# Kernel optimization log

Hardware: AMD Instinct MI355X
Metric: run time of the kernel (lower is better)

Reference implementation:

```python
import jax, jax.numpy as jnp
import numpy as np

NUM_HEADS = 4
NUM_GROUPS = 32
EPS = 1e-5

def setup_inputs() -> dict:
    key = jax.random.key(0)
    ks = jax.random.split(key, 3)
    B, C, H, W = 16, 512, 32, 32
    x = jax.random.normal(ks[0], (B, C, H, W), dtype=jnp.float32)
    gn_w = jnp.ones((C,), jnp.float32)
    gn_b = jnp.zeros((C,), jnp.float32)
    qkv_w = jax.random.normal(ks[1], (3 * C, C), dtype=jnp.float32) * (C ** -0.5)
    qkv_b = jnp.zeros((3 * C,), jnp.float32)
    proj_w = jax.random.normal(ks[2], (C, C), dtype=jnp.float32) * (C ** -0.5)
    proj_b = jnp.zeros((C,), jnp.float32)
    return {"x": x, "gn_w": gn_w, "gn_b": gn_b, "qkv_w": qkv_w,
            "qkv_b": qkv_b, "proj_w": proj_w, "proj_b": proj_b}

def group_norm(x, w, b):
    B, C, H, W = x.shape
    xg = x.reshape(B, NUM_GROUPS, C // NUM_GROUPS, H, W)
    mean = xg.mean(axis=(2, 3, 4), keepdims=True)
    var = xg.var(axis=(2, 3, 4), keepdims=True)
    xg = (xg - mean) * jax.lax.rsqrt(var + EPS)
    x = xg.reshape(B, C, H, W)
    return x * w[None, :, None, None] + b[None, :, None, None]

def reference(x, gn_w, gn_b, qkv_w, qkv_b, proj_w, proj_b):
    B, C, H, W = x.shape
    hd = C // NUM_HEADS
    h = group_norm(x, gn_w, gn_b)
    # 1x1 conv == channel matmul
    qkv = jnp.einsum('oc,bchw->bohw', qkv_w, h) + qkv_b[None, :, None, None]
    q, k, v = jnp.split(qkv, 3, axis=1)
    N = H * W
    q = q.reshape(B, NUM_HEADS, hd, N)
    k = k.reshape(B, NUM_HEADS, hd, N)
    v = v.reshape(B, NUM_HEADS, hd, N)
    scale = hd ** -0.5
    attn = jnp.einsum('bhcn,bhcm->bhnm', q, k) * scale
    attn = jax.nn.softmax(attn, axis=-1)
    o = jnp.einsum('bhnm,bhcm->bhcn', attn, v).reshape(B, C, H, W)
    o = jnp.einsum('oc,bchw->bohw', proj_w, o) + proj_b[None, :, None, None]
    return x + o
```

## Files before the change

kernel.cpp:

```cpp
#include <hip/hip_runtime.h>

typedef __attribute__((ext_vector_type(4))) float f32x4;
typedef __attribute__((ext_vector_type(8))) short s16x8;

#define MFMA16(a, b, c) __builtin_amdgcn_mfma_f32_16x16x32_bf16((a), (b), (c), 0, 0, 0)

__device__ __forceinline__ unsigned short f2bf(float f) {
    union { float f; unsigned u; } v; v.f = f;
    unsigned u = v.u + 0x7FFFu + ((v.u >> 16) & 1u);
    return (unsigned short)(u >> 16);
}

__device__ __forceinline__ unsigned cvtpk(float lo, float hi) {
    unsigned r;
    asm("v_cvt_pk_bf16_f32 %0, %1, %2" : "=v"(r) : "v"(lo), "v"(hi));
    return r;
}

__device__ __forceinline__ float exp2f_fast(float x) {
    float r;
    asm("v_exp_f32 %0, %1" : "=v"(r) : "v"(x));
    return r;
}

__device__ __forceinline__ void gll16(const unsigned short* g, unsigned short* l) {
    __builtin_amdgcn_global_load_lds((const __attribute__((address_space(1))) void*)g,
                                     (__attribute__((address_space(3))) void*)l, 16, 0, 0);
}

__global__ __launch_bounds__(256) void k_wconv(const float* __restrict__ qkv_w,
                                               const float* __restrict__ proj_w,
                                               unsigned short* __restrict__ wout) {
    int i = blockIdx.x * 256 + threadIdx.x;
    const int NQ = 3 * 512 * 512;
    float v = (i < NQ) ? qkv_w[i] : proj_w[i - NQ];
    wout[i] = f2bf(v);
}

__global__ __launch_bounds__(256) void k_gn(const float* __restrict__ x,
                                            const float* __restrict__ gnw,
                                            const float* __restrict__ gnb,
                                            unsigned short* __restrict__ h_t) {
    int bg = blockIdx.x;
    int b = bg >> 5, g = bg & 31;
    int t = threadIdx.x;
    const float4* p = (const float4*)(x + (size_t)bg * 16384);
    float s = 0.f, ss = 0.f;
    for (int i = t; i < 4096; i += 256) {
        float4 v = p[i];
        s += v.x + v.y + v.z + v.w;
        ss += v.x * v.x + v.y * v.y + v.z * v.z + v.w * v.w;
    }
    for (int w = 1; w < 64; w <<= 1) { s += __shfl_xor(s, w); ss += __shfl_xor(ss, w); }
    __shared__ float rs[4], rss[4], mv[2];
    __shared__ unsigned short ldt[1024][18];
    int wid = t >> 6;
    if ((t & 63) == 0) { rs[wid] = s; rss[wid] = ss; }
    __syncthreads();
    if (t == 0) {
        float S = rs[0] + rs[1] + rs[2] + rs[3];
        float SS = rss[0] + rss[1] + rss[2] + rss[3];
        float mean = S * (1.f / 16384.f);
        float var = SS * (1.f / 16384.f) - mean * mean;
        mv[0] = mean; mv[1] = rsqrtf(var + 1e-5f);
    }
    __syncthreads();
    int c = t >> 4, f4 = t & 15;
    float mean = mv[0], rstd = mv[1];
    float sc = gnw[g * 16 + c] * rstd;
    float sh = gnb[g * 16 + c] - mean * sc;
    const float4* pc = (const float4*)(x + ((size_t)(b * 512 + g * 16 + c)) * 1024);
#pragma unroll
    for (int i = 0; i < 16; ++i) {
        int n = i * 64 + f4 * 4;
        float4 v = pc[n >> 2];
        ldt[n + 0][c] = f2bf(v.x * sc + sh);
        ldt[n + 1][c] = f2bf(v.y * sc + sh);
        ldt[n + 2][c] = f2bf(v.z * sc + sh);
        ldt[n + 3][c] = f2bf(v.w * sc + sh);
    }
    __syncthreads();
    int half = t & 1;
#pragma unroll
    for (int i = 0; i < 8; ++i) {
        int row = i * 128 + (t >> 1);
        *(uint4*)(h_t + ((size_t)(b * 1024 + row)) * 512 + g * 16 + half * 8) =
            *(const uint4*)(&ldt[row][half * 8]);
    }
}

template<int MODE>
__global__ __launch_bounds__(512, 6) void k_gemm(const unsigned short* __restrict__ A,
                                                 const unsigned short* __restrict__ Bt,
                                                 const float* __restrict__ bias,
                                                 unsigned short* __restrict__ Qo,
                                                 unsigned short* __restrict__ Ko,
                                                 unsigned short* __restrict__ Vo,
                                                 const float* __restrict__ xres,
                                                 float* __restrict__ out) {
    const int Kd = 512;
    int id = blockIdx.x;
    int xcd = id & 7, j = id >> 3;
    int nt = xcd + 8 * (j & 15);
    int mt = j >> 4;
    int t = threadIdx.x, wid = t >> 6, lane = t & 63;
    int lm = lane & 15, q4 = lane >> 4;
    int wm = wid >> 2, wn = wid & 3;
    __shared__ unsigned short ldsA[2][4096];
    __shared__ unsigned short ldsB[2][4096];
    int m0 = mt * 128, n0 = nt * 128;

    int r = t >> 2;
    int cc = (t & 3) ^ (r & 3);
    const unsigned short* gA = A + (size_t)(m0 + r) * Kd + cc * 8;
    const unsigned short* gB = Bt + (size_t)(n0 + r) * Kd + cc * 8;
    unsigned short* dA[2] = { &ldsA[0][wid * 512], &ldsA[1][wid * 512] };
    unsigned short* dB[2] = { &ldsB[0][wid * 512], &ldsB[1][wid * 512] };

    f32x4 z = {0.f, 0.f, 0.f, 0.f};
    f32x4 acc[4][2];
#pragma unroll
    for (int fi = 0; fi < 4; ++fi)
#pragma unroll
        for (int fj = 0; fj < 2; ++fj) acc[fi][fj] = z;

    gll16(gA, dA[0]); gll16(gB, dB[0]);
    gA += 32; gB += 32;

    const int NK = 16;
    for (int ks = 0; ks < NK; ++ks) {
        int cur = ks & 1;
        if (ks + 1 < NK) {
            gll16(gA, dA[cur ^ 1]); gll16(gB, dB[cur ^ 1]);
            gA += 32; gB += 32;
            asm volatile("s_waitcnt vmcnt(2)" ::: "memory");
        } else {
            asm volatile("s_waitcnt vmcnt(0)" ::: "memory");
        }
        __builtin_amdgcn_s_barrier();
        asm volatile("" ::: "memory");
        const unsigned short* lA = ldsA[cur];
        const unsigned short* lB = ldsB[cur];
        s16x8 af[4], bg[2];
#pragma unroll
        for (int fi = 0; fi < 4; ++fi) {
            int rA = wm * 64 + fi * 16 + lm;
            af[fi] = *(const s16x8*)&lA[(rA * 4 + (q4 ^ (lm & 3))) * 8];
        }
#pragma unroll
        for (int fj = 0; fj < 2; ++fj) {
            int rB = wn * 32 + fj * 16 + lm;
            bg[fj] = *(const s16x8*)&lB[(rB * 4 + (q4 ^ (lm & 3))) * 8];
        }
        if (MODE == 0) {
#pragma unroll
            for (int fi = 0; fi < 4; ++fi)
#pragma unroll
                for (int fj = 0; fj < 2; ++fj) acc[fi][fj] = MFMA16(af[fi], bg[fj], acc[fi][fj]);
        } else {
#pragma unroll
            for (int fi = 0; fi < 4; ++fi)
#pragma unroll
                for (int fj = 0; fj < 2; ++fj) acc[fi][fj] = MFMA16(bg[fj], af[fi], acc[fi][fj]);
        }
        asm volatile("" ::: "memory");
        __builtin_amdgcn_s_barrier();
    }

    int b = nt >> 3;
    if (MODE == 0) {
        int part = mt >> 2;
        int head = mt & 3;
        int bh = b * 4 + head;
        const float qscale = 0.08838834764831845f * 1.4426950408889634f;
#pragma unroll
        for (int fi = 0; fi < 4; ++fi) {
            int ddb = wm * 64 + fi * 16 + 4 * q4;
            float bv[4];
#pragma unroll
            for (int i = 0; i < 4; ++i) bv[i] = bias[mt * 128 + ddb + i];
#pragma unroll
            for (int fj = 0; fj < 2; ++fj) {
                int n = ((nt & 7) << 7) + wn * 32 + fj * 16 + lm;
                f32x4 v = acc[fi][fj];
                uint2 pr;
                if (part == 0) {
                    pr.x = cvtpk((v[0] + bv[0]) * qscale, (v[1] + bv[1]) * qscale);
                    pr.y = cvtpk((v[2] + bv[2]) * qscale, (v[3] + bv[3]) * qscale);
                    *(uint2*)(Qo + ((size_t)bh * 1024 + n) * 128 + ddb) = pr;
                } else {
                    pr.x = cvtpk(v[0] + bv[0], v[1] + bv[1]);
                    pr.y = cvtpk(v[2] + bv[2], v[3] + bv[3]);
                    *(uint2*)(Ko + ((size_t)bh * 1024 + n) * 128 + ddb) = pr;
                }
            }
        }
    } else if (MODE == 1) {
        int bh = b * 4 + mt;
#pragma unroll
        for (int fi = 0; fi < 4; ++fi) {
            int d = wm * 64 + fi * 16 + lm;
            float bv = bias[mt * 128 + d];
#pragma unroll
            for (int fj = 0; fj < 2; ++fj) {
                int np = ((nt & 7) << 7) + wn * 32 + q4 * 8 + fj * 4;
                f32x4 v = acc[fi][fj];
                uint2 pr;
                pr.x = cvtpk(v[0] + bv, v[1] + bv);
                pr.y = cvtpk(v[2] + bv, v[3] + bv);
                *(uint2*)(Vo + ((size_t)bh * 128 + d) * 1024 + np) = pr;
            }
        }
    } else {
#pragma unroll
        for (int fi = 0; fi < 4; ++fi) {
            int oc = m0 + wm * 64 + fi * 16 + lm;
            float bv = bias[oc];
#pragma unroll
            for (int fj = 0; fj < 2; ++fj) {
                int n = ((nt & 7) << 7) + wn * 32 + fj * 16 + 4 * q4;
                size_t idx = ((size_t)b * 512 + oc) * 1024 + n;
                float4 xr = *(const float4*)&xres[idx];
                f32x4 v = acc[fi][fj];
                float4 o;
                o.x = xr.x + bv + v[0];
                o.y = xr.y + bv + v[1];
                o.z = xr.z + bv + v[2];
                o.w = xr.w + bv + v[3];
                *(float4*)&out[idx] = o;
            }
        }
    }
}

__global__ __launch_bounds__(256, 2) void k_attn(const unsigned short* __restrict__ Q,
                                                 const unsigned short* __restrict__ K,
                                                 const unsigned short* __restrict__ V,
                                                 unsigned short* __restrict__ o_t) {
    int id = blockIdx.y * 8 + blockIdx.x;
    int bh = (id & 7) + ((id >> 6) << 3);
    int qb = (id >> 3) & 7;
    int t = threadIdx.x, wid = t >> 6, lane = t & 63;
    int lm = lane & 15, q4 = lane >> 4;
    __shared__ unsigned short ldsK[2][8192];
    __shared__ unsigned short ldsV[2][8192];
    const unsigned short* Qg = Q + ((size_t)bh * 1024 + qb * 128 + wid * 32) * 128;
    const unsigned short* Kg = K + (size_t)bh * 1024 * 128;
    const unsigned short* Vg = V + (size_t)bh * 128 * 1024;

    s16x8 qf0[4], qf1[4];
#pragma unroll
    for (int dc = 0; dc < 4; ++dc) {
        qf0[dc] = *(const s16x8*)&Qg[lm * 128 + dc * 32 + q4 * 8];
        qf1[dc] = *(const s16x8*)&Qg[(16 + lm) * 128 + dc * 32 + q4 * 8];
    }

    const unsigned short* gk[4];
    const unsigned short* gv[4];
    unsigned short* lkd[2][4];
    unsigned short* lvd[2][4];
#pragma unroll
    for (int h = 0; h < 4; ++h) {
        int cib = h * 256 + wid * 64;
        int ci = cib + lane;
        int mr = ci >> 4, cl = ci & 15;
        gk[h] = Kg + mr * 128 + (cl ^ (mr & 7)) * 8;
        int d = ci >> 3, kc = ci & 7;
        gv[h] = Vg + (size_t)d * 1024 + (kc ^ (d & 7)) * 8;
        lkd[0][h] = &ldsK[0][cib * 8];
        lkd[1][h] = &ldsK[1][cib * 8];
        lvd[0][h] = &ldsV[0][cib * 8];
        lvd[1][h] = &ldsV[1][cib * 8];
    }
#pragma unroll
    for (int h = 0; h < 4; ++h) { gll16(gk[h], lkd[0][h]); gll16(gv[h], lvd[0][h]); }
#pragma unroll
    for (int h = 0; h < 4; ++h) { gk[h] += 8192; gv[h] += 64; }

    f32x4 z = {0.f, 0.f, 0.f, 0.f};
    f32x4 oa[8], ob[8];
#pragma unroll
    for (int i = 0; i < 8; ++i) { oa[i] = z; ob[i] = z; }
    float mra = -1e30f, mrb = -1e30f, lpa = 0.f, lpb = 0.f;

    auto smax = [&](const f32x4& s0a, const f32x4& s0b, const f32x4& s1a,
                    const f32x4& s1b, s16x8& fav, s16x8& fbv) {
        float tma = fmaxf(fmaxf(fmaxf(s0a[0], s0a[1]), fmaxf(s0a[2], s0a[3])),
                          fmaxf(fmaxf(s1a[0], s1a[1]), fmaxf(s1a[2], s1a[3])));
        float tmb = fmaxf(fmaxf(fmaxf(s0b[0], s0b[1]), fmaxf(s0b[2], s0b[3])),
                          fmaxf(fmaxf(s1b[0], s1b[1]), fmaxf(s1b[2], s1b[3])));
        if (!__all(tma <= mra + 8.f && tmb <= mrb + 8.f)) {
            tma = fmaxf(tma, __shfl_xor(tma, 16));
            tma = fmaxf(tma, __shfl_xor(tma, 32));
            tmb = fmaxf(tmb, __shfl_xor(tmb, 16));
            tmb = fmaxf(tmb, __shfl_xor(tmb, 32));
            float mna = fmaxf(mra, tma), mnb = fmaxf(mrb, tmb);
            float ca = exp2f_fast(mra - mna), cb = exp2f_fast(mrb - mnb);
            lpa *= ca; lpb *= cb;
#pragma unroll
            for (int t8 = 0; t8 < 8; ++t8)
#pragma unroll
                for (int i = 0; i < 4; ++i) { oa[t8][i] *= ca; ob[t8][i] *= cb; }
            mra = mna; mrb = mnb;
        }
        float pa[8], pb[8];
#pragma unroll
        for (int i = 0; i < 4; ++i) {
            pa[i]     = exp2f_fast(s0a[i] - mra);
            pa[4 + i] = exp2f_fast(s1a[i] - mra);
            pb[i]     = exp2f_fast(s0b[i] - mrb);
            pb[4 + i] = exp2f_fast(s1b[i] - mrb);
        }
#pragma unroll
        for (int i = 0; i < 8; ++i) { lpa += pa[i]; lpb += pb[i]; }
        union { s16x8 v; unsigned u[4]; } fa, fb;
        fa.u[0] = cvtpk(pa[0], pa[1]); fa.u[1] = cvtpk(pa[2], pa[3]);
        fa.u[2] = cvtpk(pa[4], pa[5]); fa.u[3] = cvtpk(pa[6], pa[7]);
        fb.u[0] = cvtpk(pb[0], pb[1]); fb.u[1] = cvtpk(pb[2], pb[3]);
        fb.u[2] = cvtpk(pb[4], pb[5]); fb.u[3] = cvtpk(pb[6], pb[7]);
        fav = fa.v; fbv = fb.v;
    };

    for (int ms = 0; ms < 16; ++ms) {
        int cur = ms & 1;
        if (ms < 15) {
            int nb = cur ^ 1;
#pragma unroll
            for (int h = 0; h < 4; ++h) { gll16(gk[h], lkd[nb][h]); gll16(gv[h], lvd[nb][h]); }
#pragma unroll
            for (int h = 0; h < 4; ++h) { gk[h] += 8192; gv[h] += 64; }
            asm volatile("s_waitcnt vmcnt(8)" ::: "memory");
        } else {
            asm volatile("s_waitcnt vmcnt(0)" ::: "memory");
        }
        __builtin_amdgcn_s_barrier();
        const unsigned short* lK = ldsK[cur];
        const unsigned short* lV = ldsV[cur];

        f32x4 sa0 = z, sb0 = z, sc0 = z, sd0 = z;
        f32x4 sa1 = z, sb1 = z, sc1 = z, sd1 = z;
        __builtin_amdgcn_s_setprio(1);
#pragma unroll
        for (int dc = 0; dc < 4; ++dc) {
            int sw = ((dc * 4 + q4) ^ (lm & 7)) * 8;
            s16x8 k0 = *(const s16x8*)&lK[lm * 128 + sw];
            s16x8 k1 = *(const s16x8*)&lK[(16 + lm) * 128 + sw];
            sa0 = MFMA16(k0, qf0[dc], sa0);
            sb0 = MFMA16(k0, qf1[dc], sb0);
            sc0 = MFMA16(k1, qf0[dc], sc0);
            sd0 = MFMA16(k1, qf1[dc], sd0);
        }
#pragma unroll
        for (int dc = 0; dc < 4; ++dc) {
            int sw = ((dc * 4 + q4) ^ (lm & 7)) * 8;
            s16x8 k0 = *(const s16x8*)&lK[(32 + lm) * 128 + sw];
            s16x8 k1 = *(const s16x8*)&lK[(48 + lm) * 128 + sw];
            sa1 = MFMA16(k0, qf0[dc], sa1);
            sb1 = MFMA16(k0, qf1[dc], sb1);
            sc1 = MFMA16(k1, qf0[dc], sc1);
            sd1 = MFMA16(k1, qf1[dc], sd1);
        }
        __builtin_amdgcn_s_setprio(0);

        s16x8 fa0, fb0;
        smax(sa0, sb0, sc0, sd0, fa0, fb0);

        __builtin_amdgcn_s_setprio(1);
#pragma unroll
        for (int t8 = 0; t8 < 8; ++t8) {
            int r = t8 * 16 + lm;
            s16x8 vf = *(const s16x8*)&lV[r * 64 + ((q4 ^ (lm & 7)) * 8)];
            oa[t8] = MFMA16(vf, fa0, oa[t8]);
            ob[t8] = MFMA16(vf, fb0, ob[t8]);
        }
        __builtin_amdgcn_s_setprio(0);

        s16x8 fa1, fb1;
        smax(sa1, sb1, sc1, sd1, fa1, fb1);

        __builtin_amdgcn_s_setprio(1);
#pragma unroll
        for (int t8 = 0; t8 < 8; ++t8) {
            int r = t8 * 16 + lm;
            s16x8 vf = *(const s16x8*)&lV[r * 64 + (((4 + q4) ^ (lm & 7)) * 8)];
            oa[t8] = MFMA16(vf, fa1, oa[t8]);
            ob[t8] = MFMA16(vf, fb1, ob[t8]);
        }
        __builtin_amdgcn_s_setprio(0);
        __builtin_amdgcn_s_barrier();
    }

    lpa += __shfl_xor(lpa, 16); lpa += __shfl_xor(lpa, 32);
    lpb += __shfl_xor(lpb, 16); lpb += __shfl_xor(lpb, 32);
    float inva = 1.f / lpa, invb = 1.f / lpb;
    int b = bh >> 2, head = bh & 3;
    size_t rowa = (size_t)b * 1024 + qb * 128 + wid * 32 + lm;
    unsigned short* da = o_t + rowa * 512 + head * 128;
    unsigned short* db = da + (size_t)16 * 512;
#pragma unroll
    for (int t8 = 0; t8 < 8; ++t8) {
        uint2 pr;
        pr.x = cvtpk(oa[t8][0] * inva, oa[t8][1] * inva);
        pr.y = cvtpk(oa[t8][2] * inva, oa[t8][3] * inva);
        *(uint2*)&da[t8 * 16 + q4 * 4] = pr;
        pr.x = cvtpk(ob[t8][0] * invb, ob[t8][1] * invb);
        pr.y = cvtpk(ob[t8][2] * invb, ob[t8][3] * invb);
        *(uint2*)&db[t8 * 16 + q4 * 4] = pr;
    }
}

extern "C" void kernel_launch(void* const* d_in, const int* in_sizes, int n_in,
                              void* d_out, int out_size, void* d_ws, size_t ws_size,
                              hipStream_t stream) {
    const float* x = (const float*)d_in[0];
    const float* gnw = (const float*)d_in[1];
    const float* gnb = (const float*)d_in[2];
    const float* qkvw = (const float*)d_in[3];
    const float* qkvb = (const float*)d_in[4];
    const float* projw = (const float*)d_in[5];
    const float* projb = (const float*)d_in[6];
    float* out = (float*)d_out;
    char* ws = (char*)d_ws;

    unsigned short* wq = (unsigned short*)(ws);
    unsigned short* wp = (unsigned short*)(ws + 1572864);
    unsigned short* ht = (unsigned short*)(ws + 2101248);
    unsigned short* Qb = (unsigned short*)(ws + 18878464);
    unsigned short* Kb = (unsigned short*)(ws + 35655680);
    unsigned short* Vb = (unsigned short*)(ws + 52432896);
    unsigned short* ot = ht;

    k_wconv<<<dim3(4096), dim3(256), 0, stream>>>(qkvw, projw, wq);
    k_gn<<<dim3(512), dim3(256), 0, stream>>>(x, gnw, gnb, ht);
    k_gemm<0><<<dim3(1024), dim3(512), 0, stream>>>(wq, ht, qkvb, Qb, Kb, nullptr, nullptr, nullptr);
    k_gemm<1><<<dim3(512), dim3(512), 0, stream>>>(wq + 8 * 128 * 512, ht, qkvb + 1024,
                                                   nullptr, nullptr, Vb, nullptr, nullptr);
    k_attn<<<dim3(8, 64), dim3(256), 0, stream>>>(Qb, Kb, Vb, ot);
    k_gemm<2><<<dim3(512), dim3(512), 0, stream>>>(wp, ot, projb, nullptr, nullptr, nullptr, x, out);
}
```

Measured before the change: 128.5 us.

## Shrink attention blocks to 64 queries and fold max subtraction into MFMA

The attention kernel now runs 128-thread blocks covering 64 query rows, with half-size K/V tiles and a 32-step KV loop, doubling the grid to 1024 blocks. The running max is preloaded into the score accumulator as a negative bias so the exponent input needs no subtraction. The row-sum is computed with an MFMA against a ones vector instead of scalar adds and cross-lane shuffles at the end. This gives more blocks for occupancy and less VALU softmax work, at the cost of more barriers, more K/V reloads per query and a smaller reuse tile.

```diff
diff --git a/kernel.cpp b/kernel.cpp
--- a/kernel.cpp
+++ b/kernel.cpp
@@ -233,18 +233,18 @@
     }
 }
 
-__global__ __launch_bounds__(256, 2) void k_attn(const unsigned short* __restrict__ Q,
+__global__ __launch_bounds__(128, 2) void k_attn(const unsigned short* __restrict__ Q,
                                                  const unsigned short* __restrict__ K,
                                                  const unsigned short* __restrict__ V,
                                                  unsigned short* __restrict__ o_t) {
     int id = blockIdx.y * 8 + blockIdx.x;
-    int bh = (id & 7) + ((id >> 6) << 3);
-    int qb = (id >> 3) & 7;
+    int bh = (id & 7) + ((id >> 7) << 3);
+    int qb = (id >> 3) & 15;
     int t = threadIdx.x, wid = t >> 6, lane = t & 63;
     int lm = lane & 15, q4 = lane >> 4;
-    __shared__ unsigned short ldsK[2][8192];
-    __shared__ unsigned short ldsV[2][8192];
-    const unsigned short* Qg = Q + ((size_t)bh * 1024 + qb * 128 + wid * 32) * 128;
+    __shared__ unsigned short ldsK[2][4096];
+    __shared__ unsigned short ldsV[2][4096];
+    const unsigned short* Qg = Q + ((size_t)bh * 1024 + qb * 64 + wid * 32) * 128;
     const unsigned short* Kg = K + (size_t)bh * 1024 * 128;
     const unsigned short* Vg = V + (size_t)bh * 128 * 1024;
 
@@ -261,12 +261,12 @@
     unsigned short* lvd[2][4];
 #pragma unroll
     for (int h = 0; h < 4; ++h) {
-        int cib = h * 256 + wid * 64;
+        int cib = h * 128 + wid * 64;
         int ci = cib + lane;
         int mr = ci >> 4, cl = ci & 15;
         gk[h] = Kg + mr * 128 + (cl ^ (mr & 7)) * 8;
-        int d = ci >> 3, kc = ci & 7;
-        gv[h] = Vg + (size_t)d * 1024 + (kc ^ (d & 7)) * 8;
+        int d = ci >> 2, kc = ci & 3;
+        gv[h] = Vg + (size_t)d * 1024 + (kc ^ ((d >> 1) & 3)) * 8;
         lkd[0][h] = &ldsK[0][cib * 8];
         lkd[1][h] = &ldsK[1][cib * 8];
         lvd[0][h] = &ldsV[0][cib * 8];
@@ -275,126 +275,103 @@
 #pragma unroll
     for (int h = 0; h < 4; ++h) { gll16(gk[h], lkd[0][h]); gll16(gv[h], lvd[0][h]); }
 #pragma unroll
-    for (int h = 0; h < 4; ++h) { gk[h] += 8192; gv[h] += 64; }
+    for (int h = 0; h < 4; ++h) { gk[h] += 4096; gv[h] += 32; }
 
     f32x4 z = {0.f, 0.f, 0.f, 0.f};
     f32x4 oa[8], ob[8];
 #pragma unroll
     for (int i = 0; i < 8; ++i) { oa[i] = z; ob[i] = z; }
-    float mra = -1e30f, mrb = -1e30f, lpa = 0.f, lpb = 0.f;
-
-    auto smax = [&](const f32x4& s0a, const f32x4& s0b, const f32x4& s1a,
-                    const f32x4& s1b, s16x8& fav, s16x8& fbv) {
-        float tma = fmaxf(fmaxf(fmaxf(s0a[0], s0a[1]), fmaxf(s0a[2], s0a[3])),
-                          fmaxf(fmaxf(s1a[0], s1a[1]), fmaxf(s1a[2], s1a[3])));
-        float tmb = fmaxf(fmaxf(fmaxf(s0b[0], s0b[1]), fmaxf(s0b[2], s0b[3])),
-                          fmaxf(fmaxf(s1b[0], s1b[1]), fmaxf(s1b[2], s1b[3])));
-        if (!__all(tma <= mra + 8.f && tmb <= mrb + 8.f)) {
+    f32x4 lca = z, lcb = z;
+    float mra = 0.f, mrb = 0.f;
+    union { s16x8 v; unsigned u[4]; } ones;
+    ones.u[0] = ones.u[1] = ones.u[2] = ones.u[3] = 0x3F803F80u;
+
+    for (int ms = 0; ms < 32; ++ms) {
+        int cur = ms & 1;
+        if (ms < 31) {
+            int nb = cur ^ 1;
+#pragma unroll
+            for (int h = 0; h < 4; ++h) { gll16(gk[h], lkd[nb][h]); gll16(gv[h], lvd[nb][h]); }
+#pragma unroll
+            for (int h = 0; h < 4; ++h) { gk[h] += 4096; gv[h] += 32; }
+            asm volatile("s_waitcnt vmcnt(8)" ::: "memory");
+        } else {
+            asm volatile("s_waitcnt vmcnt(0)" ::: "memory");
+        }
+        __builtin_amdgcn_s_barrier();
+        const unsigned short* lK = ldsK[cur];
+        const unsigned short* lV = ldsV[cur];
+
+        float nia = -mra, nib = -mrb;
+        f32x4 sa = {nia, nia, nia, nia}, sb = {nib, nib, nib, nib};
+        f32x4 sc = sa, sd = sb;
+        __builtin_amdgcn_s_setprio(1);
+#pragma unroll
+        for (int dc = 0; dc < 4; ++dc) {
+            int sw = ((dc * 4 + q4) ^ (lm & 7)) * 8;
+            s16x8 k0 = *(const s16x8*)&lK[lm * 128 + sw];
+            s16x8 k1 = *(const s16x8*)&lK[(16 + lm) * 128 + sw];
+            sa = MFMA16(k0, qf0[dc], sa);
+            sb = MFMA16(k0, qf1[dc], sb);
+            sc = MFMA16(k1, qf0[dc], sc);
+            sd = MFMA16(k1, qf1[dc], sd);
+        }
+        __builtin_amdgcn_s_setprio(0);
+
+        float tma = fmaxf(fmaxf(fmaxf(sa[0], sa[1]), fmaxf(sa[2], sa[3])),
+                          fmaxf(fmaxf(sc[0], sc[1]), fmaxf(sc[2], sc[3])));
+        float tmb = fmaxf(fmaxf(fmaxf(sb[0], sb[1]), fmaxf(sb[2], sb[3])),
+                          fmaxf(fmaxf(sd[0], sd[1]), fmaxf(sd[2], sd[3])));
+        if (!__all(tma <= 8.f && tmb <= 8.f)) {
             tma = fmaxf(tma, __shfl_xor(tma, 16));
             tma = fmaxf(tma, __shfl_xor(tma, 32));
             tmb = fmaxf(tmb, __shfl_xor(tmb, 16));
             tmb = fmaxf(tmb, __shfl_xor(tmb, 32));
-            float mna = fmaxf(mra, tma), mnb = fmaxf(mrb, tmb);
-            float ca = exp2f_fast(mra - mna), cb = exp2f_fast(mrb - mnb);
-            lpa *= ca; lpb *= cb;
+            float da_ = fmaxf(tma, 0.f), db_ = fmaxf(tmb, 0.f);
+            float ca = exp2f_fast(-da_), cb = exp2f_fast(-db_);
+            mra += da_; mrb += db_;
+#pragma unroll
+            for (int i = 0; i < 4; ++i) {
+                sa[i] -= da_; sc[i] -= da_;
+                sb[i] -= db_; sd[i] -= db_;
+            }
+            lca[0] *= ca; lcb[0] *= cb;
 #pragma unroll
             for (int t8 = 0; t8 < 8; ++t8)
 #pragma unroll
                 for (int i = 0; i < 4; ++i) { oa[t8][i] *= ca; ob[t8][i] *= cb; }
-            mra = mna; mrb = mnb;
         }
         float pa[8], pb[8];
 #pragma unroll
         for (int i = 0; i < 4; ++i) {
-            pa[i]     = exp2f_fast(s0a[i] - mra);
-            pa[4 + i] = exp2f_fast(s1a[i] - mra);
-            pb[i]     = exp2f_fast(s0b[i] - mrb);
-            pb[4 + i] = exp2f_fast(s1b[i] - mrb);
-        }
-#pragma unroll
-        for (int i = 0; i < 8; ++i) { lpa += pa[i]; lpb += pb[i]; }
+            pa[i]     = exp2f_fast(sa[i]);
+            pa[4 + i] = exp2f_fast(sc[i]);
+            pb[i]     = exp2f_fast(sb[i]);
+            pb[4 + i] = exp2f_fast(sd[i]);
+        }
         union { s16x8 v; unsigned u[4]; } fa, fb;
         fa.u[0] = cvtpk(pa[0], pa[1]); fa.u[1] = cvtpk(pa[2], pa[3]);
         fa.u[2] = cvtpk(pa[4], pa[5]); fa.u[3] = cvtpk(pa[6], pa[7]);
         fb.u[0] = cvtpk(pb[0], pb[1]); fb.u[1] = cvtpk(pb[2], pb[3]);
         fb.u[2] = cvtpk(pb[4], pb[5]); fb.u[3] = cvtpk(pb[6], pb[7]);
-        fav = fa.v; fbv = fb.v;
-    };
-
-    for (int ms = 0; ms < 16; ++ms) {
-        int cur = ms & 1;
-        if (ms < 15) {
-            int nb = cur ^ 1;
-#pragma unroll
-            for (int h = 0; h < 4; ++h) { gll16(gk[h], lkd[nb][h]); gll16(gv[h], lvd[nb][h]); }
-#pragma unroll
-            for (int h = 0; h < 4; ++h) { gk[h] += 8192; gv[h] += 64; }
-            asm volatile("s_waitcnt vmcnt(8)" ::: "memory");
-        } else {
-            asm volatile("s_waitcnt vmcnt(0)" ::: "memory");
-        }
-        __builtin_amdgcn_s_barrier();
-        const unsigned short* lK = ldsK[cur];
-        const unsigned short* lV = ldsV[cur];
-
-        f32x4 sa0 = z, sb0 = z, sc0 = z, sd0 = z;
-        f32x4 sa1 = z, sb1 = z, sc1 = z, sd1 = z;
-        __builtin_amdgcn_s_setprio(1);
-#pragma unroll
-        for (int dc = 0; dc < 4; ++dc) {
-            int sw = ((dc * 4 + q4) ^ (lm & 7)) * 8;
-            s16x8 k0 = *(const s16x8*)&lK[lm * 128 + sw];
-            s16x8 k1 = *(const s16x8*)&lK[(16 + lm) * 128 + sw];
-            sa0 = MFMA16(k0, qf0[dc], sa0);
-            sb0 = MFMA16(k0, qf1[dc], sb0);
-            sc0 = MFMA16(k1, qf0[dc], sc0);
-            sd0 = MFMA16(k1, qf1[dc], sd0);
-        }
-#pragma unroll
-        for (int dc = 0; dc < 4; ++dc) {
-            int sw = ((dc * 4 + q4) ^ (lm & 7)) * 8;
-            s16x8 k0 = *(const s16x8*)&lK[(32 + lm) * 128 + sw];
-            s16x8 k1 = *(const s16x8*)&lK[(48 + lm) * 128 + sw];
-            sa1 = MFMA16(k0, qf0[dc], sa1);
-            sb1 = MFMA16(k0, qf1[dc], sb1);
-            sc1 = MFMA16(k1, qf0[dc], sc1);
-            sd1 = MFMA16(k1, qf1[dc], sd1);
-        }
-        __builtin_amdgcn_s_setprio(0);
-
-        s16x8 fa0, fb0;
-        smax(sa0, sb0, sc0, sd0, fa0, fb0);
+        lca = MFMA16(ones.v, fa.v, lca);
+        lcb = MFMA16(ones.v, fb.v, lcb);
 
         __builtin_amdgcn_s_setprio(1);
 #pragma unroll
         for (int t8 = 0; t8 < 8; ++t8) {
             int r = t8 * 16 + lm;
-            s16x8 vf = *(const s16x8*)&lV[r * 64 + ((q4 ^ (lm & 7)) * 8)];
-            oa[t8] = MFMA16(vf, fa0, oa[t8]);
-            ob[t8] = MFMA16(vf, fb0, ob[t8]);
-        }
-        __builtin_amdgcn_s_setprio(0);
-
-        s16x8 fa1, fb1;
-        smax(sa1, sb1, sc1, sd1, fa1, fb1);
-
-        __builtin_amdgcn_s_setprio(1);
-#pragma unroll
-        for (int t8 = 0; t8 < 8; ++t8) {
-            int r = t8 * 16 + lm;
-            s16x8 vf = *(const s16x8*)&lV[r * 64 + (((4 + q4) ^ (lm & 7)) * 8)];
-            oa[t8] = MFMA16(vf, fa1, oa[t8]);
-            ob[t8] = MFMA16(vf, fb1, ob[t8]);
+            s16x8 vf = *(const s16x8*)&lV[r * 32 + ((q4 ^ ((lm >> 1) & 3)) * 8)];
+            oa[t8] = MFMA16(vf, fa.v, oa[t8]);
+            ob[t8] = MFMA16(vf, fb.v, ob[t8]);
         }
         __builtin_amdgcn_s_setprio(0);
         __builtin_amdgcn_s_barrier();
     }
 
-    lpa += __shfl_xor(lpa, 16); lpa += __shfl_xor(lpa, 32);
-    lpb += __shfl_xor(lpb, 16); lpb += __shfl_xor(lpb, 32);
-    float inva = 1.f / lpa, invb = 1.f / lpb;
+    float inva = 1.f / lca[0], invb = 1.f / lcb[0];
     int b = bh >> 2, head = bh & 3;
-    size_t rowa = (size_t)b * 1024 + qb * 128 + wid * 32 + lm;
+    size_t rowa = (size_t)b * 1024 + qb * 64 + wid * 32 + lm;
     unsigned short* da = o_t + rowa * 512 + head * 128;
     unsigned short* db = da + (size_t)16 * 512;
 #pragma unroll
@@ -435,6 +412,6 @@
     k_gemm<0><<<dim3(1024), dim3(512), 0, stream>>>(wq, ht, qkvb, Qb, Kb, nullptr, nullptr, nullptr);
     k_gemm<1><<<dim3(512), dim3(512), 0, stream>>>(wq + 8 * 128 * 512, ht, qkvb + 1024,
                                                    nullptr, nullptr, Vb, nullptr, nullptr);
-    k_attn<<<dim3(8, 64), dim3(256), 0, stream>>>(Qb, Kb, Vb, ot);
+    k_attn<<<dim3(8, 128), dim3(128), 0, stream>>>(Qb, Kb, Vb, ot);
     k_gemm<2><<<dim3(512), dim3(512), 0, stream>>>(wp, ot, projb, nullptr, nullptr, nullptr, x, out);
 }
```

Measured after the change: 134.3 us. +4.5%, slower.
